# Performance work log

Hardware: AMD Instinct MI355X
Metric: run time of the kernel (lower is better)

## Reference

```python
import jax, jax.numpy as jnp
import numpy as np

DIM = 1024
NH = 16
HD = DIM // NH
EPS = 1e-5


def setup_inputs() -> dict:
    key = jax.random.key(0)
    ks = jax.random.split(key, 6)
    B, LQ, LK = 8, 512, 1024
    s = 1.0 / np.sqrt(DIM)
    return {
        "text_tokens": jax.random.normal(ks[0], (B, LQ, DIM), dtype=jnp.float32),
        "vision_tokens": jax.random.normal(ks[1], (B, LK, DIM), dtype=jnp.float32),
        "in_proj_w": jax.random.normal(ks[2], (3 * DIM, DIM), dtype=jnp.float32) * s,
        "in_proj_b": jnp.zeros((3 * DIM,), dtype=jnp.float32),
        "out_w": jax.random.normal(ks[3], (DIM, DIM), dtype=jnp.float32) * s,
        "out_b": jnp.zeros((DIM,), dtype=jnp.float32),
        "ln_g": jnp.ones((DIM,), dtype=jnp.float32),
        "ln_b": jnp.zeros((DIM,), dtype=jnp.float32),
    }


def _layernorm(x, g, b):
    mu = jnp.mean(x, axis=-1, keepdims=True)
    var = jnp.mean(jnp.square(x - mu), axis=-1, keepdims=True)
    return (x - mu) * jax.lax.rsqrt(var + EPS) * g + b


def reference(text_tokens, vision_tokens, in_proj_w, in_proj_b, out_w, out_b, ln_g, ln_b):
    B, LQ, _ = text_tokens.shape
    LK = vision_tokens.shape[1]
    wq, wk, wv = in_proj_w[:DIM], in_proj_w[DIM:2 * DIM], in_proj_w[2 * DIM:]
    bq, bk, bv = in_proj_b[:DIM], in_proj_b[DIM:2 * DIM], in_proj_b[2 * DIM:]
    q = (text_tokens @ wq.T + bq).reshape(B, LQ, NH, HD)
    k = (vision_tokens @ wk.T + bk).reshape(B, LK, NH, HD)
    v = (vision_tokens @ wv.T + bv).reshape(B, LK, NH, HD)
    scale = 1.0 / np.sqrt(HD)
    scores = jnp.einsum("bqhd,bkhd->bhqk", q, k) * scale  # [B,H,LQ,LK]
    probs = jax.nn.softmax(scores, axis=-1)
    ctx = jnp.einsum("bhqk,bkhd->bqhd", probs, v).reshape(B, LQ, DIM)
    attended = ctx @ out_w.T + out_b
    out = _layernorm(attended + text_tokens, ln_g, ln_b)
    attn_weights = jnp.mean(probs, axis=1)  # PyTorch average_attn_weights=True
    return out, attn_weights
```

## Files before the change

kernel.cpp:

```cpp
#include <hip/hip_runtime.h>

#define DIMV 1024
#define NHV  16
#define HDV  64
#define BV   8
#define LQV  512
#define LKV  1024
#define PSTR 1032

typedef __bf16 bfrag  __attribute__((ext_vector_type(8)));
typedef float  f32x4  __attribute__((ext_vector_type(4)));
typedef unsigned short u16;
typedef unsigned int   u32;
typedef unsigned long long u64;

typedef const __attribute__((address_space(1))) u32 gu32;
typedef __attribute__((address_space(3))) u32 lu32;

__device__ __forceinline__ u16 f2bf(float f) {
    u32 x = __builtin_bit_cast(u32, f);
    x = x + 0x7FFFu + ((x >> 16) & 1u);
    return (u16)(x >> 16);
}

__device__ __forceinline__ void g2l16(const u16* g, const u16* l) {
    __builtin_amdgcn_global_load_lds(
        reinterpret_cast<gu32*>(reinterpret_cast<u64>(g)),
        reinterpret_cast<lu32*>((u32)reinterpret_cast<u64>(l)),
        16, 0, 0);
}

__global__ __launch_bounds__(256)
void cast_bf(const float* __restrict__ src, u16* __restrict__ dst, int n4)
{
    const int i = blockIdx.x * 256 + threadIdx.x;
    if (i < n4) {
        const float4 v = reinterpret_cast<const float4*>(src)[i];
        ushort4 o;
        o.x = f2bf(v.x); o.y = f2bf(v.y); o.z = f2bf(v.z); o.w = f2bf(v.w);
        reinterpret_cast<ushort4*>(dst)[i] = o;
    }
}

template<int MODE>
__global__ __launch_bounds__(256)
void gemm_nt(const u16* __restrict__ A, const u16* __restrict__ W,
             const float* __restrict__ bias, void* __restrict__ Cout,
             const float* __restrict__ resid)
{
    __shared__ __align__(16) u16 sA[128 * 64];
    __shared__ __align__(16) u16 sB[128 * 64];

    const int t    = threadIdx.x;
    const int lane = t & 63;
    const int w    = t >> 6;
    const int quad = lane >> 4;
    const int r    = lane & 15;
    const int wr   = (w >> 1) * 64;
    const int wc   = (w & 1) * 64;
    const int mb   = blockIdx.x * 128;
    const int nb   = blockIdx.y * 128;

    const int srow  = lane >> 3;
    const int skoff = (lane & 7) * 8;

    f32x4 acc[4][4] = {};

    const u16* Abase = A + (size_t)mb * 1024 + skoff;
    const u16* Wbase = W + (size_t)nb * 1024 + skoff;

    for (int k0 = 0; k0 < 1024; k0 += 64) {
#pragma unroll
        for (int it = 0; it < 4; ++it) {
            const int c = w * 4 + it;
            const int row = c * 8 + srow;
            g2l16(Abase + (size_t)row * 1024 + k0, sA + c * 512);
            g2l16(Wbase + (size_t)row * 1024 + k0, sB + c * 512);
        }
        __syncthreads();
#pragma unroll
        for (int kk = 0; kk < 2; ++kk) {
            bfrag af[4], bg[4];
#pragma unroll
            for (int i = 0; i < 4; ++i)
                af[i] = *reinterpret_cast<const bfrag*>(sA + (wr + i * 16 + r) * 64 + kk * 32 + quad * 8);
#pragma unroll
            for (int j = 0; j < 4; ++j)
                bg[j] = *reinterpret_cast<const bfrag*>(sB + (wc + j * 16 + r) * 64 + kk * 32 + quad * 8);
#pragma unroll
            for (int i = 0; i < 4; ++i)
#pragma unroll
                for (int j = 0; j < 4; ++j)
                    acc[i][j] = __builtin_amdgcn_mfma_f32_16x16x32_bf16(af[i], bg[j], acc[i][j], 0, 0, 0);
        }
        __syncthreads();
    }

#pragma unroll
    for (int i = 0; i < 4; i++)
#pragma unroll
    for (int j = 0; j < 4; j++) {
        const int colg = nb + wc + j * 16 + r;
        const float bv = bias[colg];
#pragma unroll
        for (int reg = 0; reg < 4; reg++) {
            const int rowg = mb + wr + i * 16 + quad * 4 + reg;
            const float v = acc[i][j][reg] + bv;
            if (MODE == 0) {
                ((u16*)Cout)[(size_t)rowg * 1024 + colg] = f2bf(v);
            } else if (MODE == 1) {
                ((u16*)Cout)[((size_t)((rowg >> 10) << 10) + colg) * 1024 + (rowg & 1023)] = f2bf(v);
            } else {
                ((float*)Cout)[(size_t)rowg * 1024 + colg] = v + resid[(size_t)rowg * 1024 + colg];
            }
        }
    }
}

__global__ __launch_bounds__(256, 2)
void attn_kernel(const u16* __restrict__ q, const u16* __restrict__ k,
                 const u16* __restrict__ vT, u16* __restrict__ ctx,
                 float* __restrict__ attnw)
{
    __shared__ __align__(16) u16 sP[16 * PSTR];
    __shared__ float redm[64];
    __shared__ float reds[64];

    const int t    = threadIdx.x;
    const int lane = t & 63;
    const int w    = t >> 6;
    const int quad = lane >> 4;
    const int r    = lane & 15;
    const int b    = blockIdx.y;
    const int q0   = blockIdx.x * 16;
    const int hg   = blockIdx.z;

    const int row16 = quad * 4;
    const float scale = 0.125f;

    f32x4 wacc[16] = {};

    for (int hh = 0; hh < 4; ++hh) {
        const int h = hg * 4 + hh;
        const int dbase = h * HDV + quad * 8;

        const u16* qp = q + (size_t)(b * LQV + q0 + r) * DIMV + dbase;
        const bfrag qa0 = *reinterpret_cast<const bfrag*>(qp);
        const bfrag qa1 = *reinterpret_cast<const bfrag*>(qp + 32);

        f32x4 s[16];
#pragma unroll
        for (int i = 0; i < 16; ++i) {
            const int n0 = w * 256 + i * 16;
            const u16* kp = k + (size_t)(b * LKV + n0 + r) * DIMV + dbase;
            const bfrag kb0 = *reinterpret_cast<const bfrag*>(kp);
            const bfrag kb1 = *reinterpret_cast<const bfrag*>(kp + 32);
            f32x4 a = {};
            a    = __builtin_amdgcn_mfma_f32_16x16x32_bf16(qa0, kb0, a, 0, 0, 0);
            s[i] = __builtin_amdgcn_mfma_f32_16x16x32_bf16(qa1, kb1, a, 0, 0, 0);
        }

        float mw[4] = {-1e30f, -1e30f, -1e30f, -1e30f};
#pragma unroll
        for (int i = 0; i < 16; ++i)
#pragma unroll
            for (int reg = 0; reg < 4; ++reg) {
                s[i][reg] *= scale;
                mw[reg] = fmaxf(mw[reg], s[i][reg]);
            }
#pragma unroll
        for (int reg = 0; reg < 4; ++reg)
#pragma unroll
            for (int off = 1; off < 16; off <<= 1)
                mw[reg] = fmaxf(mw[reg], __shfl_xor(mw[reg], off));

        float sw[4] = {0.f, 0.f, 0.f, 0.f};
#pragma unroll
        for (int i = 0; i < 16; ++i)
#pragma unroll
            for (int reg = 0; reg < 4; ++reg) {
                s[i][reg] = __expf(s[i][reg] - mw[reg]);
                sw[reg] += s[i][reg];
            }
#pragma unroll
        for (int reg = 0; reg < 4; ++reg)
#pragma unroll
            for (int off = 1; off < 16; off <<= 1)
                sw[reg] += __shfl_xor(sw[reg], off);

        if (r == 0) {
#pragma unroll
            for (int reg = 0; reg < 4; ++reg) {
                redm[w * 16 + row16 + reg] = mw[reg];
                reds[w * 16 + row16 + reg] = sw[reg];
            }
        }
        __syncthreads();

        float factor[4];
#pragma unroll
        for (int reg = 0; reg < 4; ++reg) {
            const int rr = row16 + reg;
            const float m0 = redm[rr], m1 = redm[16 + rr], m2 = redm[32 + rr], m3 = redm[48 + rr];
            const float M = fmaxf(fmaxf(m0, m1), fmaxf(m2, m3));
            const float total = __expf(m0 - M) * reds[rr]      + __expf(m1 - M) * reds[16 + rr] +
                                __expf(m2 - M) * reds[32 + rr] + __expf(m3 - M) * reds[48 + rr];
            factor[reg] = __expf(mw[reg] - M) / total;
        }

#pragma unroll
        for (int i = 0; i < 16; ++i)
#pragma unroll
            for (int reg = 0; reg < 4; ++reg) {
                const float pn = s[i][reg] * factor[reg];
                wacc[i][reg] += pn;
                sP[(row16 + reg) * PSTR + w * 256 + i * 16 + r] = f2bf(pn);
            }
        __syncthreads();

        {
            const int n0 = w * 16;
            f32x4 c0 = {}, c1 = {}, c2 = {}, c3 = {};
            const u16* vb = vT + (size_t)(b * DIMV + h * HDV + n0 + r) * LKV;
#pragma unroll
            for (int kk = 0; kk < LKV; kk += 128) {
                const bfrag a0 = *reinterpret_cast<const bfrag*>(&sP[r * PSTR + kk      + quad * 8]);
                const bfrag a1 = *reinterpret_cast<const bfrag*>(&sP[r * PSTR + kk + 32 + quad * 8]);
                const bfrag a2 = *reinterpret_cast<const bfrag*>(&sP[r * PSTR + kk + 64 + quad * 8]);
                const bfrag a3 = *reinterpret_cast<const bfrag*>(&sP[r * PSTR + kk + 96 + quad * 8]);
                const bfrag b0 = *reinterpret_cast<const bfrag*>(vb + kk      + quad * 8);
                const bfrag b1 = *reinterpret_cast<const bfrag*>(vb + kk + 32 + quad * 8);
                const bfrag b2 = *reinterpret_cast<const bfrag*>(vb + kk + 64 + quad * 8);
                const bfrag b3 = *reinterpret_cast<const bfrag*>(vb + kk + 96 + quad * 8);
                c0 = __builtin_amdgcn_mfma_f32_16x16x32_bf16(a0, b0, c0, 0, 0, 0);
                c1 = __builtin_amdgcn_mfma_f32_16x16x32_bf16(a1, b1, c1, 0, 0, 0);
                c2 = __builtin_amdgcn_mfma_f32_16x16x32_bf16(a2, b2, c2, 0, 0, 0);
                c3 = __builtin_amdgcn_mfma_f32_16x16x32_bf16(a3, b3, c3, 0, 0, 0);
            }
            const f32x4 c = (c0 + c1) + (c2 + c3);
#pragma unroll
            for (int reg = 0; reg < 4; ++reg)
                ctx[(size_t)(b * LQV + q0 + row16 + reg) * DIMV + h * HDV + n0 + r] = f2bf(c[reg]);
        }
        __syncthreads();
    }

    const float inv16 = 1.0f / 16.0f;
#pragma unroll
    for (int i = 0; i < 16; ++i)
#pragma unroll
        for (int reg = 0; reg < 4; ++reg)
            atomicAdd(&attnw[(size_t)(b * LQV + q0 + row16 + reg) * LKV + w * 256 + i * 16 + r],
                      wacc[i][reg] * inv16);
}

__global__ __launch_bounds__(256)
void ln_kernel(const float* __restrict__ x, const float* __restrict__ g,
               const float* __restrict__ bta, float* __restrict__ out)
{
    __shared__ float red[8];
    const int row = blockIdx.x;
    const int t = threadIdx.x;
    const int w = t >> 6;
    const float4 xv = reinterpret_cast<const float4*>(x + (size_t)row * DIMV)[t];

    float s = xv.x + xv.y + xv.z + xv.w;
#pragma unroll
    for (int off = 32; off; off >>= 1) s += __shfl_down(s, off);
    if ((t & 63) == 0) red[w] = s;
    __syncthreads();
    const float mu = (red[0] + red[1] + red[2] + red[3]) * (1.0f / 1024.0f);

    const float d0 = xv.x - mu, d1 = xv.y - mu, d2 = xv.z - mu, d3 = xv.w - mu;
    float s2 = d0 * d0 + d1 * d1 + d2 * d2 + d3 * d3;
#pragma unroll
    for (int off = 32; off; off >>= 1) s2 += __shfl_down(s2, off);
    if ((t & 63) == 0) red[4 + w] = s2;
    __syncthreads();
    const float var = (red[4] + red[5] + red[6] + red[7]) * (1.0f / 1024.0f);
    const float inv = rsqrtf(var + 1e-5f);

    float4 o;
    const int c = t * 4;
    o.x = d0 * inv * g[c + 0] + bta[c + 0];
    o.y = d1 * inv * g[c + 1] + bta[c + 1];
    o.z = d2 * inv * g[c + 2] + bta[c + 2];
    o.w = d3 * inv * g[c + 3] + bta[c + 3];
    reinterpret_cast<float4*>(out + (size_t)row * DIMV)[t] = o;
}

extern "C" void kernel_launch(void* const* d_in, const int* in_sizes, int n_in,
                              void* d_out, int out_size, void* d_ws, size_t ws_size,
                              hipStream_t stream)
{
    const float* text = (const float*)d_in[0];
    const float* vis  = (const float*)d_in[1];
    const float* wqkv = (const float*)d_in[2];
    const float* bqkv = (const float*)d_in[3];
    const float* outw = (const float*)d_in[4];
    const float* outb = (const float*)d_in[5];
    const float* lng  = (const float*)d_in[6];
    const float* lnb  = (const float*)d_in[7];

    char* ws = (char*)d_ws;
    u16*   vis_bf  = (u16*)(ws);
    u16*   ctxb    = (u16*)(ws);
    u16*   wqkv_bf = (u16*)(ws + (size_t)(16u << 20));
    u16*   outw_bf = (u16*)(ws + (size_t)(22u << 20));
    u16*   qb      = (u16*)(ws + (size_t)(24u << 20));
    u16*   text_bf = (u16*)(ws + (size_t)(32u << 20));
    u16*   kb      = (u16*)(ws + (size_t)(32u << 20));
    float* attb    = (float*)(ws + (size_t)(32u << 20));
    u16*   vTb     = (u16*)(ws + (size_t)(48u << 20));

    float* outp  = (float*)d_out;
    float* attnw = outp + (size_t)4096 * 1024;

    const dim3 blk(256);
    cast_bf<<<dim3(8192), blk, 0, stream>>>(vis,  vis_bf,  8388608 / 4);
    cast_bf<<<dim3(3072), blk, 0, stream>>>(wqkv, wqkv_bf, 3145728 / 4);
    cast_bf<<<dim3(1024), blk, 0, stream>>>(outw, outw_bf, 1048576 / 4);
    cast_bf<<<dim3(4096), blk, 0, stream>>>(text, text_bf, 4194304 / 4);

    gemm_nt<0><<<dim3(32, 8), blk, 0, stream>>>(text_bf, wqkv_bf, bqkv, qb, nullptr);
    gemm_nt<0><<<dim3(64, 8), blk, 0, stream>>>(vis_bf, wqkv_bf + DIMV * DIMV, bqkv + DIMV, kb, nullptr);
    gemm_nt<1><<<dim3(64, 8), blk, 0, stream>>>(vis_bf, wqkv_bf + 2 * DIMV * DIMV, bqkv + 2 * DIMV, vTb, nullptr);
    hipMemsetAsync(attnw, 0, (size_t)4096 * 1024 * sizeof(float), stream);
    attn_kernel<<<dim3(32, 8, 4), blk, 0, stream>>>(qb, kb, vTb, ctxb, attnw);
    gemm_nt<2><<<dim3(32, 8), blk, 0, stream>>>(ctxb, outw_bf, outb, attb, text);
    ln_kernel<<<dim3(4096), blk, 0, stream>>>(attb, lng, lnb, outp);
}
```

Baseline: 402.6 us.

## Merge head groups into one 512-thread attention block, replacing atomics and memset

Each attention block now holds two 256-thread groups that each loop over 8 heads, so one block covers all 16 heads for its 16 query rows. The head-averaged attention weights are combined through shared memory and written once with plain stores. This removes the 16 MB memset and the float atomicAdds on attnw. In exchange the grid shrinks from 1024 to 256 blocks, each doing more serial work, which cuts parallelism on a large GPU and doubles the LDS used per block.

```diff
diff --git a/kernel.cpp b/kernel.cpp
--- a/kernel.cpp
+++ b/kernel.cpp
@@ -117,31 +117,32 @@
     }
 }
 
-__global__ __launch_bounds__(256, 2)
+__global__ __launch_bounds__(512, 2)
 void attn_kernel(const u16* __restrict__ q, const u16* __restrict__ k,
                  const u16* __restrict__ vT, u16* __restrict__ ctx,
                  float* __restrict__ attnw)
 {
-    __shared__ __align__(16) u16 sP[16 * PSTR];
-    __shared__ float redm[64];
-    __shared__ float reds[64];
+    __shared__ __align__(16) u16 sP[2][16 * PSTR];
+    __shared__ float redm[2][64];
+    __shared__ float reds[2][64];
 
     const int t    = threadIdx.x;
-    const int lane = t & 63;
-    const int w    = t >> 6;
+    const int g    = t >> 8;
+    const int tg   = t & 255;
+    const int lane = tg & 63;
+    const int w    = tg >> 6;
     const int quad = lane >> 4;
     const int r    = lane & 15;
     const int b    = blockIdx.y;
     const int q0   = blockIdx.x * 16;
-    const int hg   = blockIdx.z;
 
     const int row16 = quad * 4;
     const float scale = 0.125f;
 
     f32x4 wacc[16] = {};
 
-    for (int hh = 0; hh < 4; ++hh) {
-        const int h = hg * 4 + hh;
+    for (int hh = 0; hh < 8; ++hh) {
+        const int h = g * 8 + hh;
         const int dbase = h * HDV + quad * 8;
 
         const u16* qp = q + (size_t)(b * LQV + q0 + r) * DIMV + dbase;
@@ -191,8 +192,8 @@
         if (r == 0) {
 #pragma unroll
             for (int reg = 0; reg < 4; ++reg) {
-                redm[w * 16 + row16 + reg] = mw[reg];
-                reds[w * 16 + row16 + reg] = sw[reg];
+                redm[g][w * 16 + row16 + reg] = mw[reg];
+                reds[g][w * 16 + row16 + reg] = sw[reg];
             }
         }
         __syncthreads();
@@ -201,10 +202,10 @@
 #pragma unroll
         for (int reg = 0; reg < 4; ++reg) {
             const int rr = row16 + reg;
-            const float m0 = redm[rr], m1 = redm[16 + rr], m2 = redm[32 + rr], m3 = redm[48 + rr];
+            const float m0 = redm[g][rr], m1 = redm[g][16 + rr], m2 = redm[g][32 + rr], m3 = redm[g][48 + rr];
             const float M = fmaxf(fmaxf(m0, m1), fmaxf(m2, m3));
-            const float total = __expf(m0 - M) * reds[rr]      + __expf(m1 - M) * reds[16 + rr] +
-                                __expf(m2 - M) * reds[32 + rr] + __expf(m3 - M) * reds[48 + rr];
+            const float total = __expf(m0 - M) * reds[g][rr]      + __expf(m1 - M) * reds[g][16 + rr] +
+                                __expf(m2 - M) * reds[g][32 + rr] + __expf(m3 - M) * reds[g][48 + rr];
             factor[reg] = __expf(mw[reg] - M) / total;
         }
 
@@ -214,7 +215,7 @@
             for (int reg = 0; reg < 4; ++reg) {
                 const float pn = s[i][reg] * factor[reg];
                 wacc[i][reg] += pn;
-                sP[(row16 + reg) * PSTR + w * 256 + i * 16 + r] = f2bf(pn);
+                sP[g][(row16 + reg) * PSTR + w * 256 + i * 16 + r] = f2bf(pn);
             }
         __syncthreads();
 
@@ -224,10 +225,10 @@
             const u16* vb = vT + (size_t)(b * DIMV + h * HDV + n0 + r) * LKV;
 #pragma unroll
             for (int kk = 0; kk < LKV; kk += 128) {
-                const bfrag a0 = *reinterpret_cast<const bfrag*>(&sP[r * PSTR + kk      + quad * 8]);
-                const bfrag a1 = *reinterpret_cast<const bfrag*>(&sP[r * PSTR + kk + 32 + quad * 8]);
-                const bfrag a2 = *reinterpret_cast<const bfrag*>(&sP[r * PSTR + kk + 64 + quad * 8]);
-                const bfrag a3 = *reinterpret_cast<const bfrag*>(&sP[r * PSTR + kk + 96 + quad * 8]);
+                const bfrag a0 = *reinterpret_cast<const bfrag*>(&sP[g][r * PSTR + kk      + quad * 8]);
+                const bfrag a1 = *reinterpret_cast<const bfrag*>(&sP[g][r * PSTR + kk + 32 + quad * 8]);
+                const bfrag a2 = *reinterpret_cast<const bfrag*>(&sP[g][r * PSTR + kk + 64 + quad * 8]);
+                const bfrag a3 = *reinterpret_cast<const bfrag*>(&sP[g][r * PSTR + kk + 96 + quad * 8]);
                 const bfrag b0 = *reinterpret_cast<const bfrag*>(vb + kk      + quad * 8);
                 const bfrag b1 = *reinterpret_cast<const bfrag*>(vb + kk + 32 + quad * 8);
                 const bfrag b2 = *reinterpret_cast<const bfrag*>(vb + kk + 64 + quad * 8);
@@ -245,13 +246,25 @@
         __syncthreads();
     }
 
-    const float inv16 = 1.0f / 16.0f;
-#pragma unroll
-    for (int i = 0; i < 16; ++i)
-#pragma unroll
-        for (int reg = 0; reg < 4; ++reg)
-            atomicAdd(&attnw[(size_t)(b * LQV + q0 + row16 + reg) * LKV + w * 256 + i * 16 + r],
-                      wacc[i][reg] * inv16);
+    float* cb = reinterpret_cast<float*>(&sP[0][0]);
+    if (g == 1) {
+#pragma unroll
+        for (int i = 0; i < 16; ++i)
+#pragma unroll
+            for (int reg = 0; reg < 4; ++reg)
+                cb[(i * 4 + reg) * 256 + tg] = wacc[i][reg];
+    }
+    __syncthreads();
+    if (g == 0) {
+        const float inv16 = 1.0f / 16.0f;
+#pragma unroll
+        for (int i = 0; i < 16; ++i)
+#pragma unroll
+            for (int reg = 0; reg < 4; ++reg) {
+                const float v = (wacc[i][reg] + cb[(i * 4 + reg) * 256 + tg]) * inv16;
+                attnw[(size_t)(b * LQV + q0 + row16 + reg) * LKV + w * 256 + i * 16 + r] = v;
+            }
+    }
 }
 
 __global__ __launch_bounds__(256)
@@ -325,8 +338,7 @@
     gemm_nt<0><<<dim3(32, 8), blk, 0, stream>>>(text_bf, wqkv_bf, bqkv, qb, nullptr);
     gemm_nt<0><<<dim3(64, 8), blk, 0, stream>>>(vis_bf, wqkv_bf + DIMV * DIMV, bqkv + DIMV, kb, nullptr);
     gemm_nt<1><<<dim3(64, 8), blk, 0, stream>>>(vis_bf, wqkv_bf + 2 * DIMV * DIMV, bqkv + 2 * DIMV, vTb, nullptr);
-    hipMemsetAsync(attnw, 0, (size_t)4096 * 1024 * sizeof(float), stream);
-    attn_kernel<<<dim3(32, 8, 4), blk, 0, stream>>>(qb, kb, vTb, ctxb, attnw);
+    attn_kernel<<<dim3(32, 8), dim3(512), 0, stream>>>(qb, kb, vTb, ctxb, attnw);
     gemm_nt<2><<<dim3(32, 8), blk, 0, stream>>>(ctxb, outw_bf, outb, attb, text);
     ln_kernel<<<dim3(4096), blk, 0, stream>>>(attb, lng, lnb, outp);
 }
```

Result: faster. 382.8 us (-4.9%).
